# Kernel tuning notes

Measured on AMD Instinct MI355X. Metric: run time of the kernel, lower is better.

The kernel has to match this reference:

```python
import jax, jax.numpy as jnp
import numpy as np

KS = 3          # image feature patch kernel size
RATE = 2        # downsample rate; alpha patches use kernel RATE*2, stride RATE
PENALTY = -10000.0
EPS = 1e-4
BN_EPS = 1e-5


def _pad(x, k, s):
    # reflect 'same' padding as in GCAModule.pad
    l = (k - s + 1) // 2
    r = (k - s) // 2
    return jnp.pad(x, ((0, 0), (0, 0), (l, r), (l, r)), mode='reflect')


def _extract_patches(x, k, s):
    # replicates reflect-pad + F.unfold + reshape -> (n, L, c, k, k)
    x = _pad(x, k, s)
    n, c, H, W = x.shape
    oh = (H - k) // s + 1
    ow = (W - k) // s + 1
    cols = [x[:, :, di:di + s * (oh - 1) + 1:s, dj:dj + s * (ow - 1) + 1:s]
            for di in range(k) for dj in range(k)]
    p = jnp.stack(cols, axis=2).reshape(n, c, k, k, oh * ow)  # (n,c,k,k,L)
    return jnp.transpose(p, (0, 4, 1, 2, 3))                  # (n,L,c,k,k)


def _deconv(score, kern):
    # torch: F.conv_transpose2d(score[None], kern, stride=RATE, padding=1) / 4
    # score: (L,h,w); kern: (L, ac, 4, 4) in torch conv_transpose (I,O,kh,kw) layout
    k = jnp.transpose(jnp.flip(kern, axis=(2, 3)), (1, 0, 2, 3))  # -> OIHW
    out = jax.lax.conv_general_dilated(
        score[None], k, window_strides=(1, 1), padding=[(2, 2), (2, 2)],
        lhs_dilation=(RATE, RATE), dimension_numbers=('NCHW', 'OIHW', 'NCHW'))
    return out[0] / 4.0


def gca_forward(img_feat, alpha_feat, unknown, gconv_w, gconv_b, oconv_w,
                bn_gamma, bn_beta):
    n = img_feat.shape[0]
    # guidance 1x1 conv + nearest downsample by RATE
    g = jnp.einsum('nchw,oc->nohw', img_feat, gconv_w) + gconv_b[None, :, None, None]
    g = g[:, :, ::RATE, ::RATE]
    u = unknown[:, :, ::RATE, ::RATE]
    # process_unknown_mask: per-sample softmax scales
    um = u.mean(axis=(2, 3))                                    # (n,1)
    km = 1.0 - um
    unknown_scale = jnp.clip(jnp.sqrt(um / km), 0.1, 10.0)      # (n,1)
    known_scale = jnp.clip(jnp.sqrt(km / um), 0.1, 10.0)        # (n,1)
    h, w = g.shape[2], g.shape[3]
    L = h * w
    img_ps = _extract_patches(g, KS, 1)                         # (n,L,c,3,3)
    alpha_ps = _extract_patches(alpha_feat, RATE * 2, RATE)     # (n,L,ac,4,4)
    unk_ps = _extract_patches(u, KS, 1)[:, :, 0].mean(axis=(2, 3))  # (n,L)
    # l2-normalized image patch kernels
    norm = jnp.sqrt(jnp.sum(img_ps * img_ps, axis=(2, 3, 4), keepdims=True))
    img_ps_n = img_ps / jnp.maximum(norm, EPS)
    # similarity: conv of padded g with patch kernels == patches-at-p . kernel-q
    sim = jnp.einsum('npckl,nqckl->nqp', img_ps, img_ps_n)      # (n,L,L)
    is_unknown = (unk_ps > 0.0).astype(sim.dtype)               # (n,L)
    scale = unknown_scale * is_unknown + known_scale * (1.0 - is_unknown)
    out = sim * scale[:, :, None]
    idx = jnp.arange(L)
    out = out.at[:, idx, idx].add(PENALTY * unk_ps)             # self-corr penalty
    gca = jax.nn.softmax(out, axis=1).reshape(n, L, h, w)
    prop = jax.vmap(_deconv)(gca, alpha_ps)                     # (n,ac,2h,2w)
    # out_conv: 1x1 conv (no bias) + BatchNorm (training stats) + residual
    y = jnp.einsum('nchw,oc->nohw', prop, oconv_w)
    mu = y.mean(axis=(0, 2, 3), keepdims=True)
    var = y.var(axis=(0, 2, 3), keepdims=True)
    y = (y - mu) / jnp.sqrt(var + BN_EPS)
    y = y * bn_gamma[None, :, None, None] + bn_beta[None, :, None, None]
    return y + alpha_feat


def setup_inputs():
    key = jax.random.key(0)
    ks = jax.random.split(key, 8)
    N, C, AC, H, W = 4, 256, 128, 64, 64
    img_feat = jax.random.normal(ks[0], (N, C, H, W), jnp.float32)
    alpha_feat = jax.random.normal(ks[1], (N, AC, H, W), jnp.float32)
    unknown = jax.random.randint(ks[2], (N, 1, H, W), 0, 2).astype(jnp.float32)
    gconv_w = jax.random.normal(ks[3], (C // 2, C), jnp.float32) / np.float32(np.sqrt(C))
    gconv_b = jax.random.normal(ks[4], (C // 2,), jnp.float32) * 0.01
    oconv_w = jax.random.normal(ks[5], (AC, AC), jnp.float32) / np.float32(np.sqrt(AC))
    bn_gamma = 0.001 + jax.random.normal(ks[6], (AC,), jnp.float32) * 0.001
    bn_beta = jax.random.normal(ks[7], (AC,), jnp.float32) * 0.001
    return dict(img_feat=img_feat, alpha_feat=alpha_feat, unknown=unknown,
                gconv_w=gconv_w, gconv_b=gconv_b, oconv_w=oconv_w,
                bn_gamma=bn_gamma, bn_beta=bn_beta)


def reference(img_feat, alpha_feat, unknown, gconv_w, gconv_b, oconv_w,
              bn_gamma, bn_beta):
    return gca_forward(img_feat, alpha_feat, unknown, gconv_w, gconv_b,
                       oconv_w, bn_gamma, bn_beta)
```

## Files before the change

kernel.cpp:

```cpp
#include <hip/hip_runtime.h>

#define NN 4
#define CIN 256
#define CH 128
#define HH 64
#define hh 32
#define L 1024
#define NB 2048
#define PENALTY -10000.0f
#define EPS 1e-4f

typedef __bf16 bf16x8 __attribute__((ext_vector_type(8)));
typedef float f32x4 __attribute__((ext_vector_type(4)));
typedef __attribute__((address_space(3))) void lds_t;
typedef __attribute__((address_space(1))) const void gbl_t;

__device__ __forceinline__ int refl32(int t) { return t < 0 ? -t : (t > 31 ? 62 - t : t); }
__device__ __forceinline__ int refl64(int t) { return t < 0 ? -t : (t > 63 ? 126 - t : t); }
__device__ __forceinline__ int swz(int k, int row) { return k ^ (((row >> 1) & 3) << 3); }

__global__ void k_prep(const float* __restrict__ img, const float* __restrict__ gw,
                       const float* __restrict__ ow, const float* __restrict__ unknown,
                       __bf16* __restrict__ Xb, __bf16* __restrict__ gwb,
                       __bf16* __restrict__ owb, float* __restrict__ unk,
                       float* __restrict__ scales, float* __restrict__ stats) {
    __shared__ float sm[CIN * 33];
    int bid = blockIdx.x, t = threadIdx.x;
    if (bid < 128) {
        int i = bid & 31, n = bid >> 5;
        for (int e = t; e < CIN * 16; e += 256) {
            int c = e >> 4, j2 = e & 15;
            float4 v = *(const float4*)(img + (((size_t)n * CIN + c) * HH + 2 * i) * HH + 4 * j2);
            sm[c * 33 + 2 * j2] = v.x;
            sm[c * 33 + 2 * j2 + 1] = v.z;
        }
        __syncthreads();
#pragma unroll
        for (int j = 0; j < 32; ++j) {
            int np = (n << 10) + i * 32 + j;
            int cl = swz(t, np);
            Xb[(size_t)np * CIN + t] = (__bf16)sm[cl * 33 + j];
        }
    } else if (bid < 132) {
        int n = bid - 128;
        float* u = sm;
        float* red = sm + 1024;
        float part = 0.f;
#pragma unroll
        for (int c = 0; c < 4; ++c) {
            int idx = t + c * 256;
            int i = idx >> 5, j = idx & 31;
            float v = unknown[n * 4096 + (2 * i) * HH + 2 * j];
            u[idx] = v;
            part += v;
        }
        red[t] = part;
        __syncthreads();
        for (int s = 128; s > 0; s >>= 1) {
            if (t < s) red[t] += red[t + s];
            __syncthreads();
        }
        if (t == 0) {
            float um = red[0] / 1024.0f;
            float km = 1.0f - um;
            scales[n * 2] = fminf(fmaxf(sqrtf(um / km), 0.1f), 10.0f);
            scales[n * 2 + 1] = fminf(fmaxf(sqrtf(km / um), 0.1f), 10.0f);
        }
#pragma unroll
        for (int c = 0; c < 4; ++c) {
            int idx = t + c * 256;
            int i = idx >> 5, j = idx & 31;
            float sum = 0.f;
#pragma unroll
            for (int di = -1; di <= 1; ++di)
#pragma unroll
                for (int dj = -1; dj <= 1; ++dj)
                    sum += u[refl32(i + di) * 32 + refl32(j + dj)];
            unk[n * L + idx] = sum * (1.0f / 9.0f);
        }
    } else {
        if (bid == 132) stats[t] = 0.f;
        for (int e = (bid - 132) * 256 + t; e < 49152; e += 36 * 256) {
            if (e < 32768) {
                int o = e >> 8, m = e & 255;
                gwb[e] = (__bf16)gw[o * 256 + swz(m, o)];
            } else {
                int e2 = e - 32768;
                int j = e2 >> 7, m = e2 & 127;
                owb[e2] = (__bf16)ow[j * 128 + swz(m, j)];
            }
        }
    }
}

__global__ __launch_bounds__(256, 2) void k_gemm0(const __bf16* __restrict__ Xb,
                                                  const __bf16* __restrict__ gwb,
                                                  const float* __restrict__ gb,
                                                  __bf16* __restrict__ gbf) {
    __shared__ __align__(16) __bf16 As[128 * 32];
    __shared__ __align__(16) __bf16 Bs[128 * 32];
    int p0 = blockIdx.x * 128;
    int t = threadIdx.x, l = t & 63, w = t >> 6;
    int wr = w >> 1, wc = w & 1;
    f32x4 acc[4][4] = {};
    for (int k0 = 0; k0 < CIN; k0 += 32) {
#pragma unroll
        for (int i = 0; i < 2; ++i) {
            const __bf16* srcA = Xb + (size_t)(p0 + i * 64 + (t >> 2)) * CIN + k0 + (t & 3) * 8;
            __builtin_amdgcn_global_load_lds((gbl_t*)srcA, (lds_t*)(As + i * 2048 + t * 8), 16, 0, 0);
            const __bf16* srcB = gwb + (size_t)(i * 64 + (t >> 2)) * CIN + k0 + (t & 3) * 8;
            __builtin_amdgcn_global_load_lds((gbl_t*)srcB, (lds_t*)(Bs + i * 2048 + t * 8), 16, 0, 0);
        }
        __syncthreads();
        int gl = l >> 4, r = l & 15;
        bf16x8 av[4], bv[4];
#pragma unroll
        for (int m = 0; m < 4; ++m) {
            int row = wr * 64 + m * 16 + r;
            av[m] = *(const bf16x8*)(As + row * 32 + swz(gl << 3, row));
            int col = wc * 64 + m * 16 + r;
            bv[m] = *(const bf16x8*)(Bs + col * 32 + swz(gl << 3, col));
        }
#pragma unroll
        for (int m = 0; m < 4; ++m)
#pragma unroll
            for (int c2 = 0; c2 < 4; ++c2)
                acc[m][c2] = __builtin_amdgcn_mfma_f32_16x16x32_bf16(av[m], bv[c2], acc[m][c2], 0, 0, 0);
        __syncthreads();
    }
    int r = l & 15, hi = l >> 4;
#pragma unroll
    for (int m = 0; m < 4; ++m)
#pragma unroll
        for (int c2 = 0; c2 < 4; ++c2) {
            int o = wc * 64 + c2 * 16 + r;
            float bias = gb[o];
#pragma unroll
            for (int reg = 0; reg < 4; ++reg) {
                int row = p0 + wr * 64 + m * 16 + hi * 4 + reg;
                gbf[((size_t)row << 7) + o] = (__bf16)(acc[m][c2][reg] + bias);
            }
        }
}

__global__ __launch_bounds__(256, 2) void k_gemm1(const __bf16* __restrict__ gbf,
                                                  const float* __restrict__ unk,
                                                  const float* __restrict__ scales,
                                                  const float* __restrict__ alpha,
                                                  float* __restrict__ W,
                                                  __bf16* __restrict__ Bt) {
    __shared__ __align__(16) unsigned char RAW[75008];
    int bid = blockIdx.x, t = threadIdx.x;
    if (bid >= 256) {
        float* sm = (float*)RAW;
        int blk = bid - 256;
        int n = blk >> 7, o = blk & 127;
        const float* ap = alpha + ((size_t)(n * CH + o) << 12);
#pragma unroll
        for (int j = 0; j < 4; ++j) {
            int fi = t + j * 256;
            int row = fi >> 4, c4 = fi & 15;
            float4 v = *(const float4*)(ap + fi * 4);
            float* d = sm + row * 65 + c4 * 4;
            d[0] = v.x; d[1] = v.y; d[2] = v.z; d[3] = v.w;
        }
        __syncthreads();
        __bf16* Bn = Bt + ((size_t)(n * NB) << 10);
#pragma unroll
        for (int gi = 0; gi < 8; ++gi) {
            int g = gi * 256 + t;
            int ab = g >> 7, qg = g & 127;
            int a = ab >> 2, bb = ab & 3;
            int q0 = qg * 8;
            int qi = q0 >> 5, qj0 = q0 & 31;
            int ti = refl64(2 * qi + a - 1);
            const float* r = sm + ti * 65;
            __bf16 v[8];
#pragma unroll
            for (int s = 0; s < 8; ++s) v[s] = (__bf16)r[refl64(2 * (qj0 + s) + bb - 1)];
            int j = ab * 128 + o;
            *(bf16x8*)(Bn + ((size_t)j << 10) + swz(q0, j)) = *(bf16x8*)v;
        }
        return;
    }
    __bf16* As1 = (__bf16*)RAW;
    __bf16* Bh = (__bf16*)(RAW + 49152);
    float* ssq = (float*)(RAW + 73728);
    float* ftile = ssq + 192;
    int n = bid >> 6;
    int yy = (bid >> 3) & 7, xx = bid & 7;
    int p0 = yy * 128, q0 = xx * 128;
    const __bf16* gn = gbf + ((size_t)n << 17);
    int l = t & 63, w = t >> 6;
    int wr = w >> 1, wc = w & 1;
    int by4 = yy * 4, bx4 = xx * 4;
    int rbA = by4 - 1; rbA = rbA < 0 ? 0 : (rbA > 26 ? 26 : rbA);
    int rbB = bx4 - 1; rbB = rbB < 0 ? 0 : (rbB > 26 ? 26 : rbB);
#pragma unroll
    for (int k = 0; k < 12; ++k) {
        int chunk = k / 3;
        int rem = (k % 3) * 256 + t;
        int wrow = rem >> 2, sg = rem & 3;
        int so = (chunk << 5) + ((sg ^ ((wrow >> 1) & 3)) << 3);
        int grA = ((rbA + (wrow >> 5)) << 5) + (wrow & 31);
        __builtin_amdgcn_global_load_lds((gbl_t*)(gn + (size_t)grA * 128 + so),
                                         (lds_t*)(As1 + chunk * 6144 + rem * 8), 16, 0, 0);
    }
    auto stageB = [&](int h) {
#pragma unroll
        for (int k = 0; k < 6; ++k) {
            int cl = k / 3;
            int cc = 2 * h + cl;
            int rem = (k % 3) * 256 + t;
            int wrow = rem >> 2, sg = rem & 3;
            int so = (cc << 5) + ((sg ^ ((wrow >> 1) & 3)) << 3);
            int grB = ((rbB + (wrow >> 5)) << 5) + (wrow & 31);
            __builtin_amdgcn_global_load_lds((gbl_t*)(gn + (size_t)grB * 128 + so),
                                             (lds_t*)(Bh + cl * 6144 + rem * 8), 16, 0, 0);
        }
    };
    stageB(0);
    int gl = l >> 4, r = l & 15;
    int rpA_[4][3], cpA_[4][3], rpB_[4][3], cpB_[4][3];
#pragma unroll
    for (int m = 0; m < 4; ++m) {
        int prow = wr * 64 + m * 16 + r;
        int qrow = wc * 64 + m * 16 + r;
#pragma unroll
        for (int d = 0; d < 3; ++d) {
            rpA_[m][d] = (refl32(by4 + (prow >> 5) + d - 1) - rbA) << 10;
            int cp = refl32((prow & 31) + d - 1);
            cpA_[m][d] = cp * 32 + ((gl ^ ((cp >> 1) & 3)) << 3);
            rpB_[m][d] = (refl32(bx4 + (qrow >> 5) + d - 1) - rbB) << 10;
            int cq = refl32((qrow & 31) + d - 1);
            cpB_[m][d] = cq * 32 + ((gl ^ ((cq >> 1) & 3)) << 3);
        }
    }
    f32x4 acc[4][4] = {};
    float ssqAcc = 0.f;
    auto computeH = [&](int h) {
        __builtin_amdgcn_s_setprio(1);
#pragma unroll
        for (int dk = 0; dk < 3; ++dk)
#pragma unroll
            for (int dl = 0; dl < 3; ++dl)
#pragma unroll
                for (int c = 0; c < 2; ++c) {
                    int cc = 2 * h + c;
                    bf16x8 av[4], bv[4];
#pragma unroll
                    for (int m = 0; m < 4; ++m) {
                        av[m] = *(const bf16x8*)(As1 + cc * 6144 + rpA_[m][dk] + cpA_[m][dl]);
                        bv[m] = *(const bf16x8*)(Bh + c * 6144 + rpB_[m][dk] + cpB_[m][dl]);
                    }
#pragma unroll
                    for (int m = 0; m < 4; ++m)
#pragma unroll
                        for (int c2 = 0; c2 < 4; ++c2)
                            acc[m][c2] = __builtin_amdgcn_mfma_f32_16x16x32_bf16(av[m], bv[c2], acc[m][c2], 0, 0, 0);
                }
        __builtin_amdgcn_s_setprio(0);
        if (t < 192) {
            int key = (t >> 1) & 3;
#pragma unroll
            for (int c = 0; c < 2; ++c)
#pragma unroll
                for (int g = 0; g < 4; ++g) {
                    bf16x8 v = *(const bf16x8*)(Bh + c * 6144 + t * 32 + ((g ^ key) << 3));
#pragma unroll
                    for (int u2 = 0; u2 < 8; ++u2) {
                        float x = (float)v[u2];
                        ssqAcc += x * x;
                    }
                }
        }
    };
    __syncthreads();
    computeH(0);
    __syncthreads();
    stageB(1);
    __syncthreads();
    computeH(1);
    if (t < 192) ssq[t] = ssqAcc;
    __syncthreads();
    if (t < 128) {
        int q = q0 + t;
        int qi = q >> 5, qj = q & 31;
        float sum = 0.f;
#pragma unroll
        for (int di = -1; di <= 1; ++di)
#pragma unroll
            for (int dj = -1; dj <= 1; ++dj)
                sum += ssq[(refl32(qi + di) - rbB) * 32 + refl32(qj + dj)];
        float sc = unk[n * L + q] > 0.f ? scales[n * 2] : scales[n * 2 + 1];
        ftile[t] = sc / fmaxf(sqrtf(sum), EPS);
    }
    __syncthreads();
    int hi = l >> 4;
#pragma unroll
    for (int m = 0; m < 4; ++m)
#pragma unroll
        for (int c2 = 0; c2 < 4; ++c2) {
            int q = q0 + wc * 64 + c2 * 16 + r;
            float fq = ftile[wc * 64 + c2 * 16 + r];
#pragma unroll
            for (int reg = 0; reg < 4; ++reg) {
                int p = p0 + wr * 64 + m * 16 + hi * 4 + reg;
                float val = acc[m][c2][reg] * fq;
                if (p == q) val += PENALTY * unk[n * L + p];
                W[((size_t)n << 20) + ((size_t)p << 10) + q] = val;
            }
        }
}

__global__ void k_softmax(const float* __restrict__ W, __bf16* __restrict__ Wb) {
    int t = threadIdx.x, wv = t >> 6, lane = t & 63;
    int row = blockIdx.x * 4 + wv;
    const float* Wr = W + (size_t)row * 1024;
    float v[16];
    float mx = -1e30f;
#pragma unroll
    for (int k = 0; k < 16; ++k) {
        v[k] = Wr[lane + k * 64];
        mx = fmaxf(mx, v[k]);
    }
#pragma unroll
    for (int off = 32; off > 0; off >>= 1) mx = fmaxf(mx, __shfl_xor(mx, off));
    float sum = 0.f;
#pragma unroll
    for (int k = 0; k < 16; ++k) {
        v[k] = __expf(v[k] - mx);
        sum += v[k];
    }
#pragma unroll
    for (int off = 32; off > 0; off >>= 1) sum += __shfl_xor(sum, off);
    float inv = 1.0f / sum;
    int p = row & (L - 1);
    int key = ((p >> 1) & 3) << 3;
    __bf16* Wbr = Wb + (size_t)row * 1024;
#pragma unroll
    for (int k = 0; k < 16; ++k) {
        int idx = lane + k * 64;
        Wbr[idx ^ key] = (__bf16)(v[k] * inv);
    }
}

__global__ __launch_bounds__(256, 2) void k_gemm2(const __bf16* __restrict__ Wb,
                                                  const __bf16* __restrict__ Bt,
                                                  __bf16* __restrict__ Tb) {
    int bid = blockIdx.x;
    int xcd = bid & 7, idx = bid >> 3;
    int n = xcd >> 1;
    int p0 = ((xcd & 1) * 4 + (idx & 3)) * 128;
    int j0 = (idx >> 2) * 128;
    __shared__ __align__(16) __bf16 As[4][4096];
    __shared__ __align__(16) __bf16 Bs[4][4096];
    const __bf16* An = Wb + ((size_t)n << 20);
    const __bf16* Bn = Bt + ((size_t)n * NB << 10);
    int t = threadIdx.x, l = t & 63, w = t >> 6;
    int wr = w >> 1, wc = w & 1;
    int gl = l >> 4, r = l & 15;
    f32x4 acc[4][4] = {};

    auto stage = [&](int buf, int k0) {
#pragma unroll
        for (int i = 0; i < 2; ++i) {
            int row = (t >> 2) + i * 64;
            int sgo = (t & 3) * 8;
            const __bf16* srcA = An + ((size_t)(p0 + row) << 10) + k0 + sgo;
            __builtin_amdgcn_global_load_lds((gbl_t*)srcA, (lds_t*)(&As[buf][row * 32 + sgo]), 16, 0, 0);
            const __bf16* srcB = Bn + ((size_t)(j0 + row) << 10) + k0 + sgo;
            __builtin_amdgcn_global_load_lds((gbl_t*)srcB, (lds_t*)(&Bs[buf][row * 32 + sgo]), 16, 0, 0);
        }
    };
    auto compute = [&](int buf) {
        bf16x8 av[4], bv[4];
#pragma unroll
        for (int m = 0; m < 4; ++m) {
            int row = wr * 64 + m * 16 + r;
            av[m] = *(const bf16x8*)(&As[buf][row * 32 + ((gl ^ ((row >> 1) & 3)) << 3)]);
            int col = wc * 64 + m * 16 + r;
            bv[m] = *(const bf16x8*)(&Bs[buf][col * 32 + ((gl ^ ((col >> 1) & 3)) << 3)]);
        }
#pragma unroll
        for (int m = 0; m < 4; ++m)
#pragma unroll
            for (int c2 = 0; c2 < 4; ++c2)
                acc[m][c2] = __builtin_amdgcn_mfma_f32_16x16x32_bf16(av[m], bv[c2], acc[m][c2], 0, 0, 0);
    };

    stage(0, 0);
    stage(1, 32);
    for (int it = 0; it < 32; ++it) {
        int buf = it & 3;
        if (it + 2 < 32) stage((it + 2) & 3, (it + 2) * 32);
        if (it < 30)
            asm volatile("s_waitcnt vmcnt(8)\n\ts_barrier" ::: "memory");
        else if (it == 30)
            asm volatile("s_waitcnt vmcnt(4)\n\ts_barrier" ::: "memory");
        else
            asm volatile("s_waitcnt vmcnt(0)\n\ts_barrier" ::: "memory");
        compute(buf);
    }
    int hi = l >> 4;
#pragma unroll
    for (int m = 0; m < 4; ++m)
#pragma unroll
        for (int c2 = 0; c2 < 4; ++c2) {
            int j = j0 + wc * 64 + c2 * 16 + r;
#pragma unroll
            for (int reg = 0; reg < 4; ++reg) {
                int p = p0 + wr * 64 + m * 16 + hi * 4 + reg;
                Tb[((size_t)n * L + p) * NB + j] = (__bf16)acc[m][c2][reg];
            }
        }
}

__global__ void k_oconv(const __bf16* __restrict__ owb, const __bf16* __restrict__ Tb,
                        float* __restrict__ y2, float* __restrict__ stats) {
    __shared__ __align__(16) __bf16 As[4 * 4096];
    __shared__ __align__(16) __bf16 Bp[4 * 2048];
    int n = blockIdx.z;
    int x0 = blockIdx.x * 64;
    int t = threadIdx.x, l = t & 63, w = t >> 6;
    int wr = w >> 1, wc = w & 1;
    int gl = l >> 4, r = l & 15, hi = l >> 4;
#pragma unroll
    for (int c = 0; c < 4; ++c)
#pragma unroll
        for (int i = 0; i < 2; ++i) {
            int h = i * 256 + t;
            const __bf16* src = owb + (size_t)(h >> 2) * CH + c * 32 + (h & 3) * 8;
            __builtin_amdgcn_global_load_lds((gbl_t*)src, (lds_t*)(As + c * 4096 + h * 8), 16, 0, 0);
        }
    const __bf16* Tn = Tb + ((size_t)(n * L) << 11);
#pragma unroll
    for (int it = 0; it < 4; ++it) {
        int e2 = it * 256 + t;
        int og = e2 & 15, pl = e2 >> 4;
        int pix = x0 + pl;
        int x = pix & 63, y = pix >> 6;
        float acc8[8] = {};
        int ap = (y + 1) & 1, bp = (x + 1) & 1;
#pragma unroll
        for (int da = 0; da < 2; ++da) {
            int a = ap + 2 * da;
            int ny = y + 1 - a;
            if (ny < 0 || ny >= 64) continue;
            int py = ny >> 1;
#pragma unroll
            for (int db = 0; db < 2; ++db) {
                int bb = bp + 2 * db;
                int nx = x + 1 - bb;
                if (nx < 0 || nx >= 64) continue;
                int px = nx >> 1;
                bf16x8 v = *(const bf16x8*)(Tn + (((size_t)(py * hh + px)) << 11) + (a * 4 + bb) * 128 + og * 8);
#pragma unroll
                for (int u2 = 0; u2 < 8; ++u2) acc8[u2] += (float)v[u2];
            }
        }
        __bf16 rr[8];
#pragma unroll
        for (int u2 = 0; u2 < 8; ++u2) rr[u2] = (__bf16)(acc8[u2] * 0.25f);
        int key = (pix >> 1) & 3;
        int dgl = (og & 3) ^ key;
        *(bf16x8*)(Bp + (og >> 2) * 2048 + pl * 32 + dgl * 8) = *(bf16x8*)rr;
    }
    __syncthreads();
    f32x4 acc[4][2] = {};
#pragma unroll
    for (int c = 0; c < 4; ++c) {
        bf16x8 av[4], bv[2];
#pragma unroll
        for (int m = 0; m < 4; ++m) {
            int row = wr * 64 + m * 16 + r;
            av[m] = *(const bf16x8*)(As + c * 4096 + row * 32 + ((gl ^ ((row >> 1) & 3)) << 3));
        }
#pragma unroll
        for (int c2 = 0; c2 < 2; ++c2) {
            int col = wc * 32 + c2 * 16 + r;
            bv[c2] = *(const bf16x8*)(Bp + c * 2048 + col * 32 + ((gl ^ ((col >> 1) & 3)) << 3));
        }
#pragma unroll
        for (int m = 0; m < 4; ++m)
#pragma unroll
            for (int c2 = 0; c2 < 2; ++c2)
                acc[m][c2] = __builtin_amdgcn_mfma_f32_16x16x32_bf16(av[m], bv[c2], acc[m][c2], 0, 0, 0);
    }
#pragma unroll
    for (int m = 0; m < 4; ++m)
#pragma unroll
        for (int c2 = 0; c2 < 2; ++c2) {
            int pix = x0 + wc * 32 + c2 * 16 + r;
#pragma unroll
            for (int reg = 0; reg < 4; ++reg) {
                int j = wr * 64 + m * 16 + hi * 4 + reg;
                y2[(((size_t)n * CH + j) << 12) + pix] = acc[m][c2][reg];
            }
        }
    __syncthreads();
    float* partS = (float*)As;
    float* partS2 = partS + 256;
#pragma unroll
    for (int m = 0; m < 4; ++m)
#pragma unroll
        for (int reg = 0; reg < 4; ++reg) {
            float s = 0.f, s2 = 0.f;
#pragma unroll
            for (int c2 = 0; c2 < 2; ++c2) {
                float v = acc[m][c2][reg];
                s += v;
                s2 += v * v;
            }
#pragma unroll
            for (int off = 1; off < 16; off <<= 1) {
                s += __shfl_xor(s, off);
                s2 += __shfl_xor(s2, off);
            }
            if (r == 0) {
                int j = wr * 64 + m * 16 + hi * 4 + reg;
                partS[j * 2 + wc] = s;
                partS2[j * 2 + wc] = s2;
            }
        }
    __syncthreads();
    if (t < 128) {
        atomicAdd(&stats[t * 2], partS[t * 2] + partS[t * 2 + 1]);
        atomicAdd(&stats[t * 2 + 1], partS2[t * 2] + partS2[t * 2 + 1]);
    }
}

__global__ void k_final(const float* __restrict__ y2, const float* __restrict__ stats,
                        const float* __restrict__ gamma, const float* __restrict__ beta,
                        const float* __restrict__ alpha, float* __restrict__ out) {
    int e4 = blockIdx.x * 256 + threadIdx.x;
    int oc = (e4 >> 10) & 127;
    float s1 = stats[oc * 2], s2 = stats[oc * 2 + 1];
    float mu = s1 * (1.0f / 16384.0f);
    float var = s2 * (1.0f / 16384.0f) - mu * mu;
    float inv = rsqrtf(var + 1e-5f);
    float g = gamma[oc], b = beta[oc];
    float4 yv = ((const float4*)y2)[e4];
    float4 av = ((const float4*)alpha)[e4];
    float4 o;
    o.x = (yv.x - mu) * inv * g + b + av.x;
    o.y = (yv.y - mu) * inv * g + b + av.y;
    o.z = (yv.z - mu) * inv * g + b + av.z;
    o.w = (yv.w - mu) * inv * g + b + av.w;
    ((float4*)out)[e4] = o;
}

extern "C" void kernel_launch(void* const* d_in, const int* in_sizes, int n_in,
                              void* d_out, int out_size, void* d_ws, size_t ws_size,
                              hipStream_t stream) {
    const float* img = (const float*)d_in[0];
    const float* alpha = (const float*)d_in[1];
    const float* unknown = (const float*)d_in[2];
    const float* gw = (const float*)d_in[3];
    const float* gb = (const float*)d_in[4];
    const float* ow = (const float*)d_in[5];
    const float* gamma = (const float*)d_in[6];
    const float* beta = (const float*)d_in[7];
    float* out = (float*)d_out;
    float* ws = (float*)d_ws;

    __bf16* Xb = (__bf16*)(ws);
    __bf16* gwb = (__bf16*)(ws + 524288);
    __bf16* owb = (__bf16*)(ws + 540672);
    __bf16* gbf = (__bf16*)(ws + 548864);
    float* unk = ws + 815104;
    float* scales = ws + 819200;
    float* stats = ws + 819264;
    float* W = ws + 819520;
    __bf16* Wb = (__bf16*)(ws + 5013824);
    __bf16* Bt = (__bf16*)(ws + 7110976);
    __bf16* Tb = (__bf16*)(ws + 11305280);
    float* y2 = ws + 15499584;

    k_prep<<<168, 256, 0, stream>>>(img, gw, ow, unknown, Xb, gwb, owb, unk, scales, stats);
    k_gemm0<<<32, 256, 0, stream>>>(Xb, gwb, gb, gbf);
    k_gemm1<<<768, 256, 0, stream>>>(gbf, unk, scales, alpha, W, Bt);
    k_softmax<<<1024, 256, 0, stream>>>(W, Wb);
    k_gemm2<<<512, 256, 0, stream>>>(Wb, Bt, Tb);
    k_oconv<<<dim3(64, 1, 4), 256, 0, stream>>>(owb, Tb, y2, stats);
    k_final<<<2048, 256, 0, stream>>>(y2, stats, gamma, beta, alpha, out);
}
```

Measured before the change: 91.26 us.

## Exploit Gram-matrix symmetry in k_gemm1, computing only upper-triangular tiles

The patch-correlation GEMM is symmetric up to per-column scaling, so only the 36 upper-triangular 128x128 tiles per sample are computed instead of 64. Diagonal tiles reuse the A tile in LDS as B and skip B staging. Off-diagonal tiles compute both row and column normalisation factors and write the transposed result through an LDS transpose buffer. This roughly halves MFMA work and gbf reads, at the cost of an extra LDS transpose, extra syncs and uneven per-block work.

```diff
diff --git a/kernel.cpp b/kernel.cpp
--- a/kernel.cpp
+++ b/kernel.cpp
@@ -149,11 +149,11 @@
                                                   const float* __restrict__ alpha,
                                                   float* __restrict__ W,
                                                   __bf16* __restrict__ Bt) {
-    __shared__ __align__(16) unsigned char RAW[75008];
+    __shared__ __align__(16) unsigned char RAW[76288];
     int bid = blockIdx.x, t = threadIdx.x;
-    if (bid >= 256) {
+    if (bid >= 144) {
         float* sm = (float*)RAW;
-        int blk = bid - 256;
+        int blk = bid - 144;
         int n = blk >> 7, o = blk & 127;
         const float* ap = alpha + ((size_t)(n * CH + o) << 12);
 #pragma unroll
@@ -185,10 +185,16 @@
     }
     __bf16* As1 = (__bf16*)RAW;
     __bf16* Bh = (__bf16*)(RAW + 49152);
-    float* ssq = (float*)(RAW + 73728);
-    float* ftile = ssq + 192;
-    int n = bid >> 6;
-    int yy = (bid >> 3) & 7, xx = bid & 7;
+    float* Gs = (float*)RAW;
+    float* ssqA_s = (float*)(RAW + 73728);
+    float* ssqB_s = ssqA_s + 192;
+    float* ftA = ssqA_s + 384;
+    float* ftB = ssqA_s + 512;
+    int n = bid / 36, rem = bid % 36;
+    int yy = 0;
+    while (rem >= 8 - yy) { rem -= 8 - yy; ++yy; }
+    int xx = yy + rem;
+    bool diag = (xx == yy);
     int p0 = yy * 128, q0 = xx * 128;
     const __bf16* gn = gbf + ((size_t)n << 17);
     int l = t & 63, w = t >> 6;
@@ -199,27 +205,27 @@
 #pragma unroll
     for (int k = 0; k < 12; ++k) {
         int chunk = k / 3;
-        int rem = (k % 3) * 256 + t;
-        int wrow = rem >> 2, sg = rem & 3;
+        int rem2 = (k % 3) * 256 + t;
+        int wrow = rem2 >> 2, sg = rem2 & 3;
         int so = (chunk << 5) + ((sg ^ ((wrow >> 1) & 3)) << 3);
         int grA = ((rbA + (wrow >> 5)) << 5) + (wrow & 31);
         __builtin_amdgcn_global_load_lds((gbl_t*)(gn + (size_t)grA * 128 + so),
-                                         (lds_t*)(As1 + chunk * 6144 + rem * 8), 16, 0, 0);
+                                         (lds_t*)(As1 + chunk * 6144 + rem2 * 8), 16, 0, 0);
     }
     auto stageB = [&](int h) {
 #pragma unroll
         for (int k = 0; k < 6; ++k) {
             int cl = k / 3;
             int cc = 2 * h + cl;
-            int rem = (k % 3) * 256 + t;
-            int wrow = rem >> 2, sg = rem & 3;
+            int rem2 = (k % 3) * 256 + t;
+            int wrow = rem2 >> 2, sg = rem2 & 3;
             int so = (cc << 5) + ((sg ^ ((wrow >> 1) & 3)) << 3);
             int grB = ((rbB + (wrow >> 5)) << 5) + (wrow & 31);
             __builtin_amdgcn_global_load_lds((gbl_t*)(gn + (size_t)grB * 128 + so),
-                                             (lds_t*)(Bh + cl * 6144 + rem * 8), 16, 0, 0);
+                                             (lds_t*)(Bh + cl * 6144 + rem2 * 8), 16, 0, 0);
         }
     };
-    stageB(0);
+    if (!diag) stageB(0);
     int gl = l >> 4, r = l & 15;
     int rpA_[4][3], cpA_[4][3], rpB_[4][3], cpB_[4][3];
 #pragma unroll
@@ -237,7 +243,7 @@
         }
     }
     f32x4 acc[4][4] = {};
-    float ssqAcc = 0.f;
+    float ssqAccB = 0.f;
     auto computeH = [&](int h) {
         __builtin_amdgcn_s_setprio(1);
 #pragma unroll
@@ -247,11 +253,12 @@
 #pragma unroll
                 for (int c = 0; c < 2; ++c) {
                     int cc = 2 * h + c;
+                    const __bf16* Bbase = diag ? (As1 + cc * 6144) : (Bh + c * 6144);
                     bf16x8 av[4], bv[4];
 #pragma unroll
                     for (int m = 0; m < 4; ++m) {
                         av[m] = *(const bf16x8*)(As1 + cc * 6144 + rpA_[m][dk] + cpA_[m][dl]);
-                        bv[m] = *(const bf16x8*)(Bh + c * 6144 + rpB_[m][dk] + cpB_[m][dl]);
+                        bv[m] = *(const bf16x8*)(Bbase + rpB_[m][dk] + cpB_[m][dl]);
                     }
 #pragma unroll
                     for (int m = 0; m < 4; ++m)
@@ -260,7 +267,7 @@
                             acc[m][c2] = __builtin_amdgcn_mfma_f32_16x16x32_bf16(av[m], bv[c2], acc[m][c2], 0, 0, 0);
                 }
         __builtin_amdgcn_s_setprio(0);
-        if (t < 192) {
+        if (!diag && t < 192) {
             int key = (t >> 1) & 3;
 #pragma unroll
             for (int c = 0; c < 2; ++c)
@@ -270,39 +277,73 @@
 #pragma unroll
                     for (int u2 = 0; u2 < 8; ++u2) {
                         float x = (float)v[u2];
-                        ssqAcc += x * x;
+                        ssqAccB += x * x;
                     }
                 }
         }
     };
     __syncthreads();
     computeH(0);
+    if (!diag) {
+        __syncthreads();
+        stageB(1);
+        __syncthreads();
+    }
+    computeH(1);
+    if (t < 192) {
+        float ssqAccA = 0.f;
+        int key = (t >> 1) & 3;
+#pragma unroll
+        for (int cc = 0; cc < 4; ++cc)
+#pragma unroll
+            for (int g = 0; g < 4; ++g) {
+                bf16x8 v = *(const bf16x8*)(As1 + cc * 6144 + t * 32 + ((g ^ key) << 3));
+#pragma unroll
+                for (int u2 = 0; u2 < 8; ++u2) {
+                    float x = (float)v[u2];
+                    ssqAccA += x * x;
+                }
+            }
+        ssqA_s[t] = ssqAccA;
+        if (!diag) ssqB_s[t] = ssqAccB;
+    }
     __syncthreads();
-    stageB(1);
-    __syncthreads();
-    computeH(1);
-    if (t < 192) ssq[t] = ssqAcc;
-    __syncthreads();
+    float us = scales[n * 2], ks = scales[n * 2 + 1];
     if (t < 128) {
-        int q = q0 + t;
-        int qi = q >> 5, qj = q & 31;
-        float sum = 0.f;
-#pragma unroll
-        for (int di = -1; di <= 1; ++di)
-#pragma unroll
-            for (int dj = -1; dj <= 1; ++dj)
-                sum += ssq[(refl32(qi + di) - rbB) * 32 + refl32(qj + dj)];
-        float sc = unk[n * L + q] > 0.f ? scales[n * 2] : scales[n * 2 + 1];
-        ftile[t] = sc / fmaxf(sqrtf(sum), EPS);
+        {
+            int p = p0 + t;
+            int pi = p >> 5, pj = p & 31;
+            float sum = 0.f;
+#pragma unroll
+            for (int di = -1; di <= 1; ++di)
+#pragma unroll
+                for (int dj = -1; dj <= 1; ++dj)
+                    sum += ssqA_s[(refl32(pi + di) - rbA) * 32 + refl32(pj + dj)];
+            float sc = unk[n * L + p] > 0.f ? us : ks;
+            ftA[t] = sc / fmaxf(sqrtf(sum), EPS);
+        }
+        if (!diag) {
+            int q = q0 + t;
+            int qi = q >> 5, qj = q & 31;
+            float sum = 0.f;
+#pragma unroll
+            for (int di = -1; di <= 1; ++di)
+#pragma unroll
+                for (int dj = -1; dj <= 1; ++dj)
+                    sum += ssqB_s[(refl32(qi + di) - rbB) * 32 + refl32(qj + dj)];
+            float sc = unk[n * L + q] > 0.f ? us : ks;
+            ftB[t] = sc / fmaxf(sqrtf(sum), EPS);
+        }
     }
     __syncthreads();
     int hi = l >> 4;
+    const float* fcol = diag ? ftA : ftB;
 #pragma unroll
     for (int m = 0; m < 4; ++m)
 #pragma unroll
         for (int c2 = 0; c2 < 4; ++c2) {
             int q = q0 + wc * 64 + c2 * 16 + r;
-            float fq = ftile[wc * 64 + c2 * 16 + r];
+            float fq = fcol[wc * 64 + c2 * 16 + r];
 #pragma unroll
             for (int reg = 0; reg < 4; ++reg) {
                 int p = p0 + wr * 64 + m * 16 + hi * 4 + reg;
@@ -311,6 +352,29 @@
                 W[((size_t)n << 20) + ((size_t)p << 10) + q] = val;
             }
         }
+    if (!diag) {
+        __syncthreads();
+#pragma unroll
+        for (int m = 0; m < 4; ++m)
+#pragma unroll
+            for (int c2 = 0; c2 < 4; ++c2)
+#pragma unroll
+                for (int reg = 0; reg < 4; ++reg)
+                    Gs[(wr * 64 + m * 16 + hi * 4 + reg) * 129 + wc * 64 + c2 * 16 + r] = acc[m][c2][reg];
+        __syncthreads();
+#pragma unroll
+        for (int m = 0; m < 4; ++m)
+#pragma unroll
+            for (int c2 = 0; c2 < 4; ++c2) {
+                int Cl = wc * 64 + c2 * 16 + r;
+                float fp = ftA[Cl];
+#pragma unroll
+                for (int reg = 0; reg < 4; ++reg) {
+                    int Rl = wr * 64 + m * 16 + hi * 4 + reg;
+                    W[((size_t)n << 20) + ((size_t)(q0 + Rl) << 10) + p0 + Cl] = Gs[Cl * 129 + Rl] * fp;
+                }
+            }
+    }
 }
 
 __global__ void k_softmax(const float* __restrict__ W, __bf16* __restrict__ Wb) {
@@ -579,7 +643,7 @@
 
     k_prep<<<168, 256, 0, stream>>>(img, gw, ow, unknown, Xb, gwb, owb, unk, scales, stats);
     k_gemm0<<<32, 256, 0, stream>>>(Xb, gwb, gb, gbf);
-    k_gemm1<<<768, 256, 0, stream>>>(gbf, unk, scales, alpha, W, Bt);
+    k_gemm1<<<656, 256, 0, stream>>>(gbf, unk, scales, alpha, W, Bt);
     k_softmax<<<1024, 256, 0, stream>>>(W, Wb);
     k_gemm2<<<512, 256, 0, stream>>>(Wb, Bt, Tb);
     k_oconv<<<dim3(64, 1, 4), 256, 0, stream>>>(owb, Tb, y2, stats);
```

Measured after the change: 91.93 us. About the same (+0.7%).

## Fuse prep conversion into guidance GEMM and vectorize softmax loads/stores

Applied to the files above, without the earlier changes.

Merges the preprocessing kernel into the guidance 1x1-conv GEMM. Each block now converts its own fp32 image tile and the full guidance weight to bf16 directly into shared memory, which removes the Xb/gwb intermediate buffers and one kernel launch. Mask statistics and the oconv weight conversion move into extra blocks of the same launch. Softmax also switches to float4 loads and packed bf16 stores. The tradeoffs are a strided, uncoalesced fp32 gather of the image with a redundant per-block weight conversion, and 72KB of shared memory per block.

```diff
diff --git a/kernel.cpp b/kernel.cpp
--- a/kernel.cpp
+++ b/kernel.cpp
@@ -19,32 +19,30 @@
 __device__ __forceinline__ int refl64(int t) { return t < 0 ? -t : (t > 63 ? 126 - t : t); }
 __device__ __forceinline__ int swz(int k, int row) { return k ^ (((row >> 1) & 3) << 3); }
 
-__global__ void k_prep(const float* __restrict__ img, const float* __restrict__ gw,
-                       const float* __restrict__ ow, const float* __restrict__ unknown,
-                       __bf16* __restrict__ Xb, __bf16* __restrict__ gwb,
-                       __bf16* __restrict__ owb, float* __restrict__ unk,
-                       float* __restrict__ scales, float* __restrict__ stats) {
-    __shared__ float sm[CIN * 33];
+__global__ __launch_bounds__(256, 2) void k_gemm0(const float* __restrict__ img,
+                                                  const float* __restrict__ gw,
+                                                  const float* __restrict__ gb,
+                                                  const float* __restrict__ unknown,
+                                                  const float* __restrict__ ow,
+                                                  __bf16* __restrict__ gbf,
+                                                  __bf16* __restrict__ owb,
+                                                  float* __restrict__ unk,
+                                                  float* __restrict__ scales,
+                                                  float* __restrict__ stats) {
+    __shared__ __align__(16) unsigned char RAW[73728];
     int bid = blockIdx.x, t = threadIdx.x;
-    if (bid < 128) {
-        int i = bid & 31, n = bid >> 5;
-        for (int e = t; e < CIN * 16; e += 256) {
-            int c = e >> 4, j2 = e & 15;
-            float4 v = *(const float4*)(img + (((size_t)n * CIN + c) * HH + 2 * i) * HH + 4 * j2);
-            sm[c * 33 + 2 * j2] = v.x;
-            sm[c * 33 + 2 * j2 + 1] = v.z;
-        }
-        __syncthreads();
-#pragma unroll
-        for (int j = 0; j < 32; ++j) {
-            int np = (n << 10) + i * 32 + j;
-            int cl = swz(t, np);
-            Xb[(size_t)np * CIN + t] = (__bf16)sm[cl * 33 + j];
-        }
-    } else if (bid < 132) {
-        int n = bid - 128;
-        float* u = sm;
-        float* red = sm + 1024;
+    if (bid >= 36) {
+        for (int e = (bid - 36) * 256 + t; e < 16384; e += 8 * 256) {
+            int j = e >> 7, m = e & 127;
+            owb[e] = (__bf16)ow[j * 128 + swz(m, j)];
+        }
+        return;
+    }
+    if (bid >= 32) {
+        if (bid == 32) stats[t] = 0.f;
+        int n = bid - 32;
+        float* u = (float*)RAW;
+        float* red = u + 1024;
         float part = 0.f;
 #pragma unroll
         for (int c = 0; c < 4; ++c) {
@@ -78,38 +76,41 @@
                     sum += u[refl32(i + di) * 32 + refl32(j + dj)];
             unk[n * L + idx] = sum * (1.0f / 9.0f);
         }
-    } else {
-        if (bid == 132) stats[t] = 0.f;
-        for (int e = (bid - 132) * 256 + t; e < 49152; e += 36 * 256) {
-            if (e < 32768) {
-                int o = e >> 8, m = e & 255;
-                gwb[e] = (__bf16)gw[o * 256 + swz(m, o)];
-            } else {
-                int e2 = e - 32768;
-                int j = e2 >> 7, m = e2 & 127;
-                owb[e2] = (__bf16)ow[j * 128 + swz(m, j)];
-            }
-        }
-    }
-}
-
-__global__ __launch_bounds__(256, 2) void k_gemm0(const __bf16* __restrict__ Xb,
-                                                  const __bf16* __restrict__ gwb,
-                                                  const float* __restrict__ gb,
-                                                  __bf16* __restrict__ gbf) {
-    __shared__ __align__(16) __bf16 As[128 * 32];
-    __shared__ __align__(16) __bf16 Bs[128 * 32];
-    int p0 = blockIdx.x * 128;
-    int t = threadIdx.x, l = t & 63, w = t >> 6;
+        return;
+    }
+    __bf16* Bfull = (__bf16*)RAW;
+    __bf16* As = (__bf16*)(RAW + 65536);
+    int p0 = bid * 128;
+    int n = bid >> 3;
+    int ib = (bid & 7) << 2;
+    int l = t & 63, w = t >> 6;
     int wr = w >> 1, wc = w & 1;
+#pragma unroll
+    for (int it = 0; it < 16; ++it) {
+        int fg = it * 256 + t;
+        int o = fg >> 5, sg = fg & 31;
+        const float* src = gw + o * 256 + sg * 8;
+        __bf16 v[8];
+#pragma unroll
+        for (int e = 0; e < 8; ++e) v[e] = (__bf16)src[e];
+        int cs = sg >> 2, lg = sg & 3;
+        int dg = lg ^ ((o >> 1) & 3);
+        *(bf16x8*)(Bfull + o * 256 + (cs * 4 + dg) * 8) = *(bf16x8*)v;
+    }
     f32x4 acc[4][4] = {};
     for (int k0 = 0; k0 < CIN; k0 += 32) {
 #pragma unroll
-        for (int i = 0; i < 2; ++i) {
-            const __bf16* srcA = Xb + (size_t)(p0 + i * 64 + (t >> 2)) * CIN + k0 + (t & 3) * 8;
-            __builtin_amdgcn_global_load_lds((gbl_t*)srcA, (lds_t*)(As + i * 2048 + t * 8), 16, 0, 0);
-            const __bf16* srcB = gwb + (size_t)(i * 64 + (t >> 2)) * CIN + k0 + (t & 3) * 8;
-            __builtin_amdgcn_global_load_lds((gbl_t*)srcB, (lds_t*)(Bs + i * 2048 + t * 8), 16, 0, 0);
+        for (int gi = 0; gi < 2; ++gi) {
+            int row = t & 127;
+            int sg = (t >> 7) + gi * 2;
+            int i = ib + (row >> 5), j = row & 31;
+            int c0 = k0 + sg * 8;
+            const float* ip = img + (((size_t)n * CIN + c0) * HH + 2 * i) * HH + 2 * j;
+            __bf16 v[8];
+#pragma unroll
+            for (int e = 0; e < 8; ++e) v[e] = (__bf16)ip[(size_t)e * HH * HH];
+            int dg = sg ^ ((row >> 1) & 3);
+            *(bf16x8*)(As + row * 32 + dg * 8) = *(bf16x8*)v;
         }
         __syncthreads();
         int gl = l >> 4, r = l & 15;
@@ -119,7 +120,7 @@
             int row = wr * 64 + m * 16 + r;
             av[m] = *(const bf16x8*)(As + row * 32 + swz(gl << 3, row));
             int col = wc * 64 + m * 16 + r;
-            bv[m] = *(const bf16x8*)(Bs + col * 32 + swz(gl << 3, col));
+            bv[m] = *(const bf16x8*)(Bfull + col * 256 + k0 + swz(gl << 3, col));
         }
 #pragma unroll
         for (int m = 0; m < 4; ++m)
@@ -316,21 +317,24 @@
 __global__ void k_softmax(const float* __restrict__ W, __bf16* __restrict__ Wb) {
     int t = threadIdx.x, wv = t >> 6, lane = t & 63;
     int row = blockIdx.x * 4 + wv;
-    const float* Wr = W + (size_t)row * 1024;
-    float v[16];
+    const float4* Wr4 = (const float4*)(W + (size_t)row * 1024);
+    float4 v[4];
     float mx = -1e30f;
 #pragma unroll
-    for (int k = 0; k < 16; ++k) {
-        v[k] = Wr[lane + k * 64];
-        mx = fmaxf(mx, v[k]);
+    for (int k = 0; k < 4; ++k) {
+        v[k] = Wr4[lane + k * 64];
+        mx = fmaxf(mx, fmaxf(fmaxf(v[k].x, v[k].y), fmaxf(v[k].z, v[k].w)));
     }
 #pragma unroll
     for (int off = 32; off > 0; off >>= 1) mx = fmaxf(mx, __shfl_xor(mx, off));
     float sum = 0.f;
 #pragma unroll
-    for (int k = 0; k < 16; ++k) {
-        v[k] = __expf(v[k] - mx);
-        sum += v[k];
+    for (int k = 0; k < 4; ++k) {
+        v[k].x = __expf(v[k].x - mx);
+        v[k].y = __expf(v[k].y - mx);
+        v[k].z = __expf(v[k].z - mx);
+        v[k].w = __expf(v[k].w - mx);
+        sum += (v[k].x + v[k].y) + (v[k].z + v[k].w);
     }
 #pragma unroll
     for (int off = 32; off > 0; off >>= 1) sum += __shfl_xor(sum, off);
@@ -339,9 +343,16 @@
     int key = ((p >> 1) & 3) << 3;
     __bf16* Wbr = Wb + (size_t)row * 1024;
 #pragma unroll
-    for (int k = 0; k < 16; ++k) {
-        int idx = lane + k * 64;
-        Wbr[idx ^ key] = (__bf16)(v[k] * inv);
+    for (int k = 0; k < 4; ++k) {
+        int base = 4 * lane + 256 * k;
+        __bf16 o4[4];
+        o4[0] = (__bf16)(v[k].x * inv);
+        o4[1] = (__bf16)(v[k].y * inv);
+        o4[2] = (__bf16)(v[k].z * inv);
+        o4[3] = (__bf16)(v[k].w * inv);
+        __bf16* dst = Wbr + (base ^ key);
+        *(uint*)dst = *(uint*)&o4[0];
+        *(uint*)(dst + 2) = *(uint*)&o4[2];
     }
 }
 
@@ -564,8 +575,6 @@
     float* out = (float*)d_out;
     float* ws = (float*)d_ws;
 
-    __bf16* Xb = (__bf16*)(ws);
-    __bf16* gwb = (__bf16*)(ws + 524288);
     __bf16* owb = (__bf16*)(ws + 540672);
     __bf16* gbf = (__bf16*)(ws + 548864);
     float* unk = ws + 815104;
@@ -577,8 +586,7 @@
     __bf16* Tb = (__bf16*)(ws + 11305280);
     float* y2 = ws + 15499584;
 
-    k_prep<<<168, 256, 0, stream>>>(img, gw, ow, unknown, Xb, gwb, owb, unk, scales, stats);
-    k_gemm0<<<32, 256, 0, stream>>>(Xb, gwb, gb, gbf);
+    k_gemm0<<<44, 256, 0, stream>>>(img, gw, gb, unknown, ow, gbf, owb, unk, scales, stats);
     k_gemm1<<<768, 256, 0, stream>>>(gbf, unk, scales, alpha, W, Bt);
     k_softmax<<<1024, 256, 0, stream>>>(W, Wb);
     k_gemm2<<<512, 256, 0, stream>>>(Wb, Bt, Tb);
```

Result: no change. 91.32 us (+0.1%).
